# Kernel optimization log

Hardware: AMD Instinct MI355X
Metric: run time of the kernel (lower is better)

Reference implementation:

```python
import jax, jax.numpy as jnp
import numpy as np

B, S, H = 2, 1024, 4096
NH, NKV, HD = 32, 8, 128
GROUPS = NH // NKV  # 4


def _dequant_linear(x, w_q, scale, bias=None):
    # torch Linear layout: W [out, in]; per-output-channel symmetric dequant
    w = w_q.astype(jnp.float32) * scale[:, None]
    y = jnp.einsum('bsi,oi->bso', x, w)
    if bias is not None:
        y = y + bias
    return y


def setup_inputs() -> dict:
    key = jax.random.key(0)
    ks = jax.random.split(key, 12)
    hidden_states = jax.random.normal(ks[0], (B, S, H), dtype=jnp.float32)
    # additive causal mask: 0 on/below diagonal, large negative above
    causal = jnp.where(jnp.tril(jnp.ones((S, S), dtype=bool)), 0.0, -1e9).astype(jnp.float32)
    attention_mask = jnp.broadcast_to(causal[None, None], (B, 1, S, S))
    # int8-valued quantized weights, per-out-channel scales (~unit-variance effective weight rows / sqrt(fan_in))
    def qw(k, out, inp):
        return jax.random.randint(k, (out, inp), -127, 128, dtype=jnp.int32)
    def sc(k, out):
        return jax.random.uniform(k, (out,), dtype=jnp.float32, minval=1e-4, maxval=3e-4)
    wq_q = qw(ks[1], H, H);            wq_s = sc(ks[2], H)
    wk_q = qw(ks[3], NKV * HD, H);     wk_s = sc(ks[4], NKV * HD)
    wv_q = qw(ks[5], NKV * HD, H);     wv_s = sc(ks[6], NKV * HD)
    wo_q = qw(ks[7], H, H);            wo_s = sc(ks[8], H)
    bq = jax.random.normal(ks[9], (H,), dtype=jnp.float32) * 0.02
    bk = jax.random.normal(ks[10], (NKV * HD,), dtype=jnp.float32) * 0.02
    return {
        'hidden_states': hidden_states, 'attention_mask': attention_mask,
        'wq_q': wq_q, 'wq_s': wq_s, 'bq': bq,
        'wk_q': wk_q, 'wk_s': wk_s, 'bk': bk,
        'wv_q': wv_q, 'wv_s': wv_s,
        'wo_q': wo_q, 'wo_s': wo_s,
    }


def reference(hidden_states, attention_mask, wq_q, wq_s, bq, wk_q, wk_s, bk, wv_q, wv_s, wo_q, wo_s):
    bsz, q_len, _ = hidden_states.shape
    q = _dequant_linear(hidden_states, wq_q, wq_s, bq)      # [B,S,H]
    k = _dequant_linear(hidden_states, wk_q, wk_s, bk)      # [B,S,NKV*HD]
    v = _dequant_linear(hidden_states, wv_q, wv_s)          # [B,S,NKV*HD]
    q = q.reshape(bsz, q_len, NH, HD).transpose(0, 2, 1, 3)     # [B,NH,S,HD]
    k = k.reshape(bsz, q_len, NKV, HD).transpose(0, 2, 1, 3)    # [B,NKV,S,HD]
    v = v.reshape(bsz, q_len, NKV, HD).transpose(0, 2, 1, 3)
    # GQA: repeat_interleave kv heads along head dim
    k = jnp.repeat(k, GROUPS, axis=1)   # [B,NH,S,HD]
    v = jnp.repeat(v, GROUPS, axis=1)
    scores = jnp.einsum('bhqd,bhkd->bhqk', q, k) / np.float32(np.sqrt(HD))
    scores = scores + attention_mask
    attn = jax.nn.softmax(scores.astype(jnp.float32), axis=-1).astype(q.dtype)
    out = jnp.einsum('bhqk,bhkd->bhqd', attn, v)            # [B,NH,S,HD]
    out = out.transpose(0, 2, 1, 3).reshape(bsz, q_len, H)
    out = _dequant_linear(out, wo_q, wo_s)
    return out
```

## Files before the change

kernel.cpp:

```cpp
#include <hip/hip_runtime.h>
#include <math.h>

#define BB   2
#define SS   1024
#define HH   4096
#define NHH  32
#define NKVV 8
#define HDD  128
#define MR   2048
#define KVD  1024
#define NQKVD 6144
#define KD   4096
#define KHALF 2048
#define SCALE_F 0.08838834764831845f

typedef __attribute__((ext_vector_type(8))) short bf16x8;
typedef __attribute__((ext_vector_type(4))) float f32x4;
typedef __attribute__((ext_vector_type(4))) int i32x4;

#define MFMA(a, b, c) __builtin_amdgcn_mfma_f32_16x16x32_bf16((a), (b), (c), 0, 0, 0)
#define MFMA_I8(a, b, c) __builtin_amdgcn_mfma_i32_16x16x64_i8((a), (b), (c), 0, 0, 0)

__device__ __forceinline__ unsigned short f2bf(float f) {
  union { float f; unsigned u; } v; v.f = f;
  return (unsigned short)((v.u + 0x7fffu + ((v.u >> 16) & 1u)) >> 16);
}
__device__ __forceinline__ unsigned short f2h(float f) {
  union { _Float16 h; unsigned short s; } v; v.h = (_Float16)f; return v.s;
}
__device__ __forceinline__ float h2f(unsigned short s) {
  union { unsigned short s; _Float16 h; } v; v.s = s; return (float)v.h;
}
__device__ __forceinline__ float bf2f(unsigned short s) {
  union { unsigned u; float f; } v; v.u = ((unsigned)s) << 16; return v.f;
}
__device__ __forceinline__ float4 ld4h(const unsigned short* p) {
  uint2 d = *(const uint2*)p;
  float4 r;
  r.x = h2f((unsigned short)(d.x & 0xffff)); r.y = h2f((unsigned short)(d.x >> 16));
  r.z = h2f((unsigned short)(d.y & 0xffff)); r.w = h2f((unsigned short)(d.y >> 16));
  return r;
}

__device__ __forceinline__ void gload_lds16(const void* g, void* l) {
  __builtin_amdgcn_global_load_lds(
      (const __attribute__((address_space(1))) void*)g,
      (__attribute__((address_space(3))) void*)l, 16, 0, 0);
}

__device__ __forceinline__ signed char q8(float x, float inv) {
  float r = rintf(x * inv);
  r = fmaxf(-127.f, fminf(127.f, r));
  return (signed char)(int)r;
}

#define NQ16 ((size_t)HH * HH / 16)
#define NK16 ((size_t)KVD * HH / 16)
__global__ void cvt_w_all(const int* __restrict__ wq, const int* __restrict__ wk,
                          const int* __restrict__ wv, const int* __restrict__ wo,
                          signed char* __restrict__ wqkv, signed char* __restrict__ wo8) {
  size_t i = (size_t)blockIdx.x * 256 + threadIdx.x;
  const int* src;
  signed char* dst;
  if (i < NQ16) { src = wq; dst = wqkv; }
  else if (i < NQ16 + NK16) { src = wk - NQ16 * 16; dst = wqkv; }
  else if (i < NQ16 + 2 * NK16) { src = wv - (NQ16 + NK16) * 16; dst = wqkv; }
  else { src = wo - (NQ16 + 2 * NK16) * 16; dst = wo8 - (NQ16 + 2 * NK16) * 16; }
  const int4* p = (const int4*)(src + i * 16);
  union { signed char c[16]; int4 q; } o;
#pragma unroll
  for (int j = 0; j < 4; ++j) {
    int4 v = p[j];
    o.c[j * 4 + 0] = (signed char)v.x; o.c[j * 4 + 1] = (signed char)v.y;
    o.c[j * 4 + 2] = (signed char)v.z; o.c[j * 4 + 3] = (signed char)v.w;
  }
  *(int4*)(dst + i * 16) = o.q;
}

__global__ void quant_f32(const float* __restrict__ in, signed char* __restrict__ out,
                          float* __restrict__ scale) {
  __shared__ float wm[4];
  const int row = blockIdx.x;
  const int t = threadIdx.x;
  const float4* p = (const float4*)(in + (size_t)row * HH) + t * 4;
  float4 v[4];
  float m = 0.f;
#pragma unroll
  for (int j = 0; j < 4; ++j) {
    v[j] = p[j];
    m = fmaxf(m, fmaxf(fmaxf(fabsf(v[j].x), fabsf(v[j].y)), fmaxf(fabsf(v[j].z), fabsf(v[j].w))));
  }
#pragma unroll
  for (int o = 32; o; o >>= 1) m = fmaxf(m, __shfl_xor(m, o));
  if ((t & 63) == 0) wm[t >> 6] = m;
  __syncthreads();
  m = fmaxf(fmaxf(wm[0], wm[1]), fmaxf(wm[2], wm[3]));
  m = fmaxf(m, 1e-12f);
  const float inv = 127.f / m;
  union { signed char c[16]; int4 q; } o;
#pragma unroll
  for (int j = 0; j < 4; ++j) {
    o.c[j * 4 + 0] = q8(v[j].x, inv); o.c[j * 4 + 1] = q8(v[j].y, inv);
    o.c[j * 4 + 2] = q8(v[j].z, inv); o.c[j * 4 + 3] = q8(v[j].w, inv);
  }
  ((int4*)(out + (size_t)row * HH))[t] = o.q;
  if (t == 0) scale[row] = m / 127.f;
}

__global__ void quant_bf16(const unsigned short* __restrict__ in, signed char* __restrict__ out,
                           float* __restrict__ scale) {
  __shared__ float wm[4];
  const int row = blockIdx.x;
  const int t = threadIdx.x;
  const uint4* p = (const uint4*)(in + (size_t)row * HH) + t * 2;
  float f[16];
  float m = 0.f;
#pragma unroll
  for (int j = 0; j < 2; ++j) {
    uint4 d = p[j];
    unsigned u[4] = {d.x, d.y, d.z, d.w};
#pragma unroll
    for (int k = 0; k < 4; ++k) {
      f[j * 8 + k * 2] = bf2f((unsigned short)(u[k] & 0xffff));
      f[j * 8 + k * 2 + 1] = bf2f((unsigned short)(u[k] >> 16));
    }
  }
#pragma unroll
  for (int e = 0; e < 16; ++e) m = fmaxf(m, fabsf(f[e]));
#pragma unroll
  for (int o = 32; o; o >>= 1) m = fmaxf(m, __shfl_xor(m, o));
  if ((t & 63) == 0) wm[t >> 6] = m;
  __syncthreads();
  m = fmaxf(fmaxf(wm[0], wm[1]), fmaxf(wm[2], wm[3]));
  m = fmaxf(m, 1e-12f);
  const float inv = 127.f / m;
  union { signed char c[16]; int4 q; } o;
#pragma unroll
  for (int e = 0; e < 16; ++e) o.c[e] = q8(f[e], inv);
  ((int4*)(out + (size_t)row * HH))[t] = o.q;
  if (t == 0) scale[row] = m / 127.f;
}

template <int MODE>
__global__ __launch_bounds__(256) void gemm_i8(
    const signed char* __restrict__ A, const signed char* __restrict__ W,
    const float* __restrict__ sRow,
    const float* __restrict__ s0, const float* __restrict__ s1, const float* __restrict__ s2,
    unsigned short* __restrict__ P, int N) {
  __shared__ signed char ldsA[128 * 128];
  __shared__ signed char ldsB[128 * 128];
  const int t = threadIdx.x;
  const int lane = t & 63;
  const int w = t >> 6;
  const int wr = w & 1, wc = w >> 1;
  const int l15 = lane & 15, quad = lane >> 4;
  const int bm = blockIdx.y, bn = blockIdx.x, kz = blockIdx.z;

  const int srow_ = t >> 3;
  const int scol_ = ((t & 7) ^ (srow_ & 7)) * 16;
  const signed char* gA = A + (size_t)(bm * 128 + srow_) * KD + scol_ + kz * KHALF;
  const signed char* gW = W + (size_t)(bn * 128 + srow_) * KD + scol_ + kz * KHALF;
  signed char* lA = ldsA + t * 16;
  signed char* lB = ldsB + t * 16;

  i32x4 acc[4][4] = {};

  for (int k0 = 0; k0 < KHALF; k0 += 128) {
    __syncthreads();
#pragma unroll
    for (int j = 0; j < 4; ++j) {
      gload_lds16(gA + (size_t)j * 32 * KD + k0, lA + j * 4096);
      gload_lds16(gW + (size_t)j * 32 * KD + k0, lB + j * 4096);
    }
    __syncthreads();
#pragma unroll
    for (int kc = 0; kc < 2; ++kc) {
      i32x4 af[4], bfr[4];
#pragma unroll
      for (int mi = 0; mi < 4; ++mi) {
        const int row = wr * 64 + mi * 16 + l15;
        const int ch = (kc * 4 + quad) ^ (row & 7);
        af[mi] = *(const i32x4*)(ldsA + row * 128 + ch * 16);
      }
#pragma unroll
      for (int ni = 0; ni < 4; ++ni) {
        const int row = wc * 64 + ni * 16 + l15;
        const int ch = (kc * 4 + quad) ^ (row & 7);
        bfr[ni] = *(const i32x4*)(ldsB + row * 128 + ch * 16);
      }
#pragma unroll
      for (int mi = 0; mi < 4; ++mi)
#pragma unroll
        for (int ni = 0; ni < 4; ++ni)
          acc[mi][ni] = MFMA_I8(af[mi], bfr[ni], acc[mi][ni]);
    }
  }

  unsigned short* Pz = P + (size_t)kz * MR * N;
  const int row0 = bm * 128 + wr * 64 + quad * 4;
  const int col0 = bn * 128 + wc * 64 + l15;
#pragma unroll
  for (int ni = 0; ni < 4; ++ni) {
    const int col = col0 + ni * 16;
    float sc;
    if (MODE == 0)
      sc = (col < HH) ? s0[col] : (col < HH + KVD) ? s1[col - HH] : s2[col - HH - KVD];
    else
      sc = s0[col];
#pragma unroll
    for (int mi = 0; mi < 4; ++mi)
#pragma unroll
      for (int r = 0; r < 4; ++r) {
        const int row = row0 + mi * 16 + r;
        const float v = (float)acc[mi][ni][r] * sRow[row] * sc;
        Pz[(size_t)row * N + col] = f2h(v);
      }
  }
}

__global__ void epi_qkv(const unsigned short* __restrict__ P0, const unsigned short* __restrict__ P1,
                        const float* __restrict__ bQ, const float* __restrict__ bK,
                        unsigned short* __restrict__ oQ, unsigned short* __restrict__ oK,
                        unsigned short* __restrict__ oVt) {
  __shared__ unsigned short lds_t[64][65];
  const int t = threadIdx.x;
  int bid = blockIdx.x;
  if (bid < 10240) {
    const int row = bid / 5;
    const int col = (bid - row * 5) * 1024 + t * 4;
    const size_t off = (size_t)row * NQKVD + col;
    float4 a = ld4h(P0 + off), b2 = ld4h(P1 + off);
    union { unsigned short s[4]; uint2 d; } o;
    if (col < HH) {
      const float4 b = *(const float4*)(bQ + col);
      o.s[0] = f2bf((a.x + b2.x + b.x) * SCALE_F);
      o.s[1] = f2bf((a.y + b2.y + b.y) * SCALE_F);
      o.s[2] = f2bf((a.z + b2.z + b.z) * SCALE_F);
      o.s[3] = f2bf((a.w + b2.w + b.w) * SCALE_F);
      *(uint2*)(oQ + (size_t)row * HH + col) = o.d;
    } else {
      const int c = col - HH;
      const float4 b = *(const float4*)(bK + c);
      o.s[0] = f2bf(a.x + b2.x + b.x); o.s[1] = f2bf(a.y + b2.y + b.y);
      o.s[2] = f2bf(a.z + b2.z + b.z); o.s[3] = f2bf(a.w + b2.w + b.w);
      *(uint2*)(oK + (size_t)row * KVD + c) = o.d;
    }
  } else {
    bid -= 10240;
    const int c0 = (bid & 15) * 64;
    const int r0 = (bid >> 4) * 64;
    const int c4 = (t & 15) * 4;
#pragma unroll
    for (int rr = 0; rr < 4; ++rr) {
      const int rl = (t >> 4) * 4 + rr;
      const size_t off = (size_t)(r0 + rl) * NQKVD + (HH + KVD) + c0 + c4;
      float4 a = ld4h(P0 + off), b = ld4h(P1 + off);
      lds_t[c4 + 0][rl] = f2bf(a.x + b.x);
      lds_t[c4 + 1][rl] = f2bf(a.y + b.y);
      lds_t[c4 + 2][rl] = f2bf(a.z + b.z);
      lds_t[c4 + 3][rl] = f2bf(a.w + b.w);
    }
    __syncthreads();
    const int cl = t >> 2;
    const int rs = (t & 3) * 16;
    union { unsigned short s[16]; uint4 q[2]; } o;
#pragma unroll
    for (int i = 0; i < 16; ++i) o.s[i] = lds_t[cl][rs + i];
    uint4* dst = (uint4*)(oVt + (size_t)(c0 + cl) * MR + r0 + rs);
    dst[0] = o.q[0]; dst[1] = o.q[1];
  }
}

__global__ void epi_o(const unsigned short* __restrict__ P0, const unsigned short* __restrict__ P1,
                      float* __restrict__ out) {
  const int col = (blockIdx.x * 256 + threadIdx.x) * 4;
  const int row = blockIdx.y;
  const size_t off = (size_t)row * HH + col;
  float4 a = ld4h(P0 + off), b = ld4h(P1 + off);
  *(float4*)(out + off) = make_float4(a.x + b.x, a.y + b.y, a.z + b.z, a.w + b.w);
}

__global__ __launch_bounds__(256, 3) void attn_kernel(
    const unsigned short* __restrict__ Q,
    const unsigned short* __restrict__ K,
    const unsigned short* __restrict__ Vt,
    unsigned short* __restrict__ O) {
  __shared__ unsigned short ldsK[4 * 64 * 32];
  __shared__ unsigned short ldsV[2 * 128 * 32];
  __shared__ unsigned short ldsP[4][16 * 88];
  const int t = threadIdx.x;
  const int lane = t & 63;
  const int wv = t >> 6;
  const int l15 = lane & 15, quad = lane >> 4;
  const int qt = 15 - blockIdx.x;
  const int h = blockIdx.y;
  const int b = blockIdx.z;
  const int kv = h >> 2;
  const int q0w = qt * 64 + wv * 16;
  const int q = q0w + l15;

  bf16x8 bq[4];
  const unsigned short* qbase = Q + (size_t)(b * SS + q0w + l15) * HH + h * HDD + quad * 8;
#pragma unroll
  for (int kk = 0; kk < 4; ++kk) bq[kk] = *(const bf16x8*)(qbase + kk * 32);

  const unsigned short* gK = K + (size_t)(b * SS) * KVD + kv * HDD + wv * 32 + (lane & 3) * 8;
  const unsigned short* gV = Vt + (size_t)(kv * HDD + wv * 32 + (lane >> 2)) * MR + b * SS + (lane & 3) * 8;
  unsigned short* lK = ldsK + wv * 2048 + lane * 8;
  unsigned short* lV = ldsV + (size_t)wv * 32 * 32 + lane * 8;
  unsigned short* lp = ldsP[wv];

  f32x4 accO[8] = {};
  float m_run = -1e30f, l_run = 0.f;

  for (int kt = 0; kt <= qt; ++kt) {
    const int k0 = kt * 64;
    __syncthreads();
#pragma unroll
    for (int j = 0; j < 4; ++j)
      gload_lds16(gK + (size_t)(k0 + j * 16 + (lane >> 2)) * KVD, lK + j * 512);
#pragma unroll
    for (int kc = 0; kc < 2; ++kc)
#pragma unroll
      for (int j = 0; j < 2; ++j)
        gload_lds16(gV + (size_t)j * 16 * MR + k0 + kc * 32,
                    lV + kc * 4096 + j * 512);
    __syncthreads();

    f32x4 st[4] = {};
#pragma unroll
    for (int kk = 0; kk < 4; ++kk)
#pragma unroll
      for (int mf = 0; mf < 4; ++mf) {
        bf16x8 af = *(const bf16x8*)(ldsK + kk * 2048 + (mf * 16 + l15) * 32 + quad * 8);
        st[mf] = MFMA(af, bq[kk], st[mf]);
      }

    float p[4][4];
    float cm = -1e30f;
#pragma unroll
    for (int mf = 0; mf < 4; ++mf)
#pragma unroll
      for (int r = 0; r < 4; ++r) {
        const int k = k0 + mf * 16 + quad * 4 + r;
        float v = st[mf][r];
        if (k > q) v = -1e30f;
        p[mf][r] = v;
        cm = fmaxf(cm, v);
      }
    cm = fmaxf(cm, __shfl_xor(cm, 16));
    cm = fmaxf(cm, __shfl_xor(cm, 32));
    const float mn = fmaxf(m_run, cm);
    const float al = __expf(m_run - mn);
    float sum = 0.f;
#pragma unroll
    for (int mf = 0; mf < 4; ++mf)
#pragma unroll
      for (int r = 0; r < 4; ++r) {
        const float e = __expf(p[mf][r] - mn);
        p[mf][r] = e;
        sum += e;
      }
    sum += __shfl_xor(sum, 16);
    sum += __shfl_xor(sum, 32);
    l_run = l_run * al + sum;
    m_run = mn;
    float af4[4];
#pragma unroll
    for (int r = 0; r < 4; ++r) af4[r] = __shfl(al, quad * 4 + r);
#pragma unroll
    for (int cb = 0; cb < 8; ++cb)
#pragma unroll
      for (int r = 0; r < 4; ++r) accO[cb][r] *= af4[r];

#pragma unroll
    for (int mf = 0; mf < 4; ++mf) {
      union { unsigned short s[4]; unsigned long long d; } pk;
#pragma unroll
      for (int r = 0; r < 4; ++r) pk.s[r] = f2bf(p[mf][r]);
      *(unsigned long long*)(lp + l15 * 88 + mf * 16 + quad * 4) = pk.d;
    }
    bf16x8 ap0 = *(const bf16x8*)(lp + l15 * 88 + quad * 8);
    bf16x8 ap1 = *(const bf16x8*)(lp + l15 * 88 + 32 + quad * 8);

#pragma unroll
    for (int cb = 0; cb < 8; ++cb) {
      bf16x8 bv0 = *(const bf16x8*)(ldsV + (cb * 16 + l15) * 32 + quad * 8);
      bf16x8 bv1 = *(const bf16x8*)(ldsV + 4096 + (cb * 16 + l15) * 32 + quad * 8);
      accO[cb] = MFMA(ap0, bv0, accO[cb]);
      accO[cb] = MFMA(ap1, bv1, accO[cb]);
    }
  }

  float lr[4];
#pragma unroll
  for (int r = 0; r < 4; ++r) lr[r] = __shfl(l_run, quad * 4 + r);
  unsigned short* ob = O + (size_t)(b * SS + q0w + quad * 4) * HH + h * HDD + l15;
#pragma unroll
  for (int cb = 0; cb < 8; ++cb)
#pragma unroll
    for (int r = 0; r < 4; ++r)
      ob[(size_t)r * HH + cb * 16] = f2bf(accO[cb][r] / lr[r]);
}

extern "C" void kernel_launch(void* const* d_in, const int* in_sizes, int n_in,
                              void* d_out, int out_size, void* d_ws, size_t ws_size,
                              hipStream_t stream) {
  const float* x = (const float*)d_in[0];
  const int* wq = (const int*)d_in[2];
  const float* wqs = (const float*)d_in[3];
  const float* bq = (const float*)d_in[4];
  const int* wk = (const int*)d_in[5];
  const float* wks = (const float*)d_in[6];
  const float* bk = (const float*)d_in[7];
  const int* wv = (const int*)d_in[8];
  const float* wvs = (const float*)d_in[9];
  const int* wo = (const int*)d_in[10];
  const float* wos = (const float*)d_in[11];
  float* out = (float*)d_out;
  char* ws = (char*)d_ws;

  signed char*    x_i8    = (signed char*)   (ws + (0ull   << 20));
  signed char*    wqkv_i8 = (signed char*)   (ws + (8ull   << 20));
  signed char*    wo_i8   = (signed char*)   (ws + (32ull  << 20));
  unsigned short* Pq      = (unsigned short*)(ws + (48ull  << 20));
  unsigned short* q_bf    = (unsigned short*)(ws + (0ull   << 20));
  unsigned short* k_bf    = (unsigned short*)(ws + (16ull  << 20));
  unsigned short* v_t     = (unsigned short*)(ws + (20ull  << 20));
  unsigned short* a_bf    = (unsigned short*)(ws + (48ull  << 20));
  signed char*    a_i8    = (signed char*)   (ws + (64ull  << 20));
  unsigned short* Po      = (unsigned short*)(ws + (96ull  << 20));
  float*          sx      = (float*)         (ws + (128ull << 20));
  float*          sa      = (float*)         (ws + (129ull << 20));
  if (ws_size < (130ull << 20)) return;

  quant_f32<<<MR, 256, 0, stream>>>(x, x_i8, sx);
  cvt_w_all<<<10240, 256, 0, stream>>>(wq, wk, wv, wo, wqkv_i8, wo_i8);

  gemm_i8<0><<<dim3(NQKVD / 128, MR / 128, 2), 256, 0, stream>>>(
      x_i8, wqkv_i8, sx, wqs, wks, wvs, Pq, NQKVD);

  epi_qkv<<<10752, 256, 0, stream>>>(Pq, Pq + (size_t)MR * NQKVD, bq, bk, q_bf, k_bf, v_t);

  attn_kernel<<<dim3(16, NHH, BB), 256, 0, stream>>>(q_bf, k_bf, v_t, a_bf);

  quant_bf16<<<MR, 256, 0, stream>>>(a_bf, a_i8, sa);
  gemm_i8<1><<<dim3(HH / 128, MR / 128, 2), 256, 0, stream>>>(
      a_i8, wo_i8, sa, wos, nullptr, nullptr, Po, HH);
  epi_o<<<dim3(4, MR), 256, 0, stream>>>(Po, Po + (size_t)MR * HH, out);
}
```

Baseline: 428.1 us.

## Double-buffer K tiles in LDS and read V directly from global memory

The attention kernel now keeps K tiles in a two-stage LDS ring buffer with an XOR-swizzled row layout. The next K tile is prefetched while the current one is computed, and only one barrier per iteration remains. V tiles are no longer staged through LDS; each wave loads its V fragments straight from global (Vt), relying on L2/L1 reuse across the waves and heads that share a KV group. This aims to overlap loads with compute and cut LDS bank conflicts, at the cost of redundant global V reads per wave and exposed global latency inside the PV MFMA loop.

```diff
diff --git a/kernel.cpp b/kernel.cpp
--- a/kernel.cpp
+++ b/kernel.cpp
@@ -285,8 +285,7 @@
     const unsigned short* __restrict__ K,
     const unsigned short* __restrict__ Vt,
     unsigned short* __restrict__ O) {
-  __shared__ unsigned short ldsK[4 * 64 * 32];
-  __shared__ unsigned short ldsV[2 * 128 * 32];
+  __shared__ unsigned short ldsK[2][64][128];
   __shared__ unsigned short ldsP[4][16 * 88];
   const int t = threadIdx.x;
   const int lane = t & 63;
@@ -304,35 +303,37 @@
 #pragma unroll
   for (int kk = 0; kk < 4; ++kk) bq[kk] = *(const bf16x8*)(qbase + kk * 32);
 
-  const unsigned short* gK = K + (size_t)(b * SS) * KVD + kv * HDD + wv * 32 + (lane & 3) * 8;
-  const unsigned short* gV = Vt + (size_t)(kv * HDD + wv * 32 + (lane >> 2)) * MR + b * SS + (lane & 3) * 8;
-  unsigned short* lK = ldsK + wv * 2048 + lane * 8;
-  unsigned short* lV = ldsV + (size_t)wv * 32 * 32 + lane * 8;
+  const int srow = t >> 4;
+  const int schunk = (t & 15) ^ (srow & 7);
+  const unsigned short* gK = K + (size_t)(b * SS + srow) * KVD + kv * HDD + schunk * 8;
   unsigned short* lp = ldsP[wv];
+  const unsigned short* vb = Vt + (size_t)(kv * HDD + l15) * MR + b * SS + quad * 8;
 
   f32x4 accO[8] = {};
   float m_run = -1e30f, l_run = 0.f;
 
+#pragma unroll
+  for (int j = 0; j < 4; ++j)
+    gload_lds16(gK + (size_t)j * 16 * KVD, &ldsK[0][j * 16][0] + t * 8);
+  __syncthreads();
+
+  int cur = 0;
   for (int kt = 0; kt <= qt; ++kt) {
     const int k0 = kt * 64;
-    __syncthreads();
-#pragma unroll
-    for (int j = 0; j < 4; ++j)
-      gload_lds16(gK + (size_t)(k0 + j * 16 + (lane >> 2)) * KVD, lK + j * 512);
-#pragma unroll
-    for (int kc = 0; kc < 2; ++kc)
-#pragma unroll
-      for (int j = 0; j < 2; ++j)
-        gload_lds16(gV + (size_t)j * 16 * MR + k0 + kc * 32,
-                    lV + kc * 4096 + j * 512);
-    __syncthreads();
+    if (kt < qt) {
+#pragma unroll
+      for (int j = 0; j < 4; ++j)
+        gload_lds16(gK + (size_t)(k0 + 64 + j * 16) * KVD,
+                    &ldsK[cur ^ 1][j * 16][0] + t * 8);
+    }
 
     f32x4 st[4] = {};
 #pragma unroll
     for (int kk = 0; kk < 4; ++kk)
 #pragma unroll
       for (int mf = 0; mf < 4; ++mf) {
-        bf16x8 af = *(const bf16x8*)(ldsK + kk * 2048 + (mf * 16 + l15) * 32 + quad * 8);
+        const int r = mf * 16 + l15;
+        bf16x8 af = *(const bf16x8*)(&ldsK[cur][r][((kk * 4 + quad) ^ (r & 7)) * 8]);
         st[mf] = MFMA(af, bq[kk], st[mf]);
       }
 
@@ -385,11 +386,14 @@
 
 #pragma unroll
     for (int cb = 0; cb < 8; ++cb) {
-      bf16x8 bv0 = *(const bf16x8*)(ldsV + (cb * 16 + l15) * 32 + quad * 8);
-      bf16x8 bv1 = *(const bf16x8*)(ldsV + 4096 + (cb * 16 + l15) * 32 + quad * 8);
+      bf16x8 bv0 = *(const bf16x8*)(vb + (size_t)cb * 16 * MR + k0);
+      bf16x8 bv1 = *(const bf16x8*)(vb + (size_t)cb * 16 * MR + k0 + 32);
       accO[cb] = MFMA(ap0, bv0, accO[cb]);
       accO[cb] = MFMA(ap1, bv1, accO[cb]);
     }
+
+    __syncthreads();
+    cur ^= 1;
   }
 
   float lr[4];
```

Measured after the change: 497.7 us. 16.2% more time.
